# Performance work log

Measured on AMD Instinct MI355X. Metric: run time of the kernel, lower is better.

The kernel has to match this reference:

```python
import jax, jax.numpy as jnp
import numpy as np

B, T, N, PRED, DM = 16, 512, 128, 256, 32
L = T + PRED  # 768; conv windows 12 then 4: 768 -> 64 -> 16
EPS = 1e-5


def _conv1d(x, w, b, stride):
    # x: [B, C, L'], w: [C, C, k], kernel_size == stride, VALID (matches torch Conv1d)
    out = jax.lax.conv_general_dilated(x, w, (stride,), 'VALID',
                                       dimension_numbers=('NCH', 'OIH', 'NCH'))
    return out + b[None, :, None]


def _conv2d(x, w, b, pad):
    out = jax.lax.conv_general_dilated(x, w, (1, 1), [(pad, pad), (pad, pad)],
                                       dimension_numbers=('NCHW', 'OIHW', 'NCHW'))
    return out + b[None, :, None, None]


def _bn1d(x, g, b):
    # BatchNorm1d, training-mode batch statistics over (batch, length) per channel
    mu = x.mean((0, 2), keepdims=True)
    var = ((x - mu) ** 2).mean((0, 2), keepdims=True)
    return (x - mu) * jax.lax.rsqrt(var + EPS) * g[None, :, None] + b[None, :, None]


def _cubic_spline(y, size):
    # Natural cubic spline through values y: [B, Lk, C] at knots t = linspace(0,1,Lk),
    # evaluated at linspace(0,1,size). Natural BC: second derivative M=0 at endpoints.
    Bb, Lk, C = y.shape
    h = 1.0 / (Lk - 1)
    # tridiagonal system for interior second derivatives (uniform knots):
    # M[i-1] + 4 M[i] + M[i+1] = 6 * (y[i+1] - 2 y[i] + y[i-1]) / h^2
    m = Lk - 2
    rhs = (y[:, 2:, :] - 2.0 * y[:, 1:-1, :] + y[:, :-2, :]) * (6.0 / (h * h))  # [B,m,C]
    A = 4.0 * jnp.eye(m, dtype=y.dtype) + jnp.eye(m, k=1, dtype=y.dtype) + jnp.eye(m, k=-1, dtype=y.dtype)
    Mi = jnp.linalg.solve(A, rhs.transpose(1, 0, 2).reshape(m, Bb * C))  # [m, B*C]
    Mi = Mi.reshape(m, Bb, C).transpose(1, 0, 2)
    M = jnp.pad(Mi, ((0, 0), (1, 1), (0, 0)))  # [B, Lk, C], M[0]=M[-1]=0
    q = jnp.linspace(0.0, 1.0, size).astype(y.dtype)
    idx = jnp.clip(jnp.floor(q * (Lk - 1)).astype(jnp.int32), 0, Lk - 2)  # [size]
    s = (q - idx.astype(y.dtype) * h)[None, :, None]  # offset within interval
    u = h - s
    yi, yi1 = y[:, idx, :], y[:, idx + 1, :]
    M0, M1 = M[:, idx, :], M[:, idx + 1, :]
    hh6 = h * h / 6.0
    return ((M0 * u ** 3 + M1 * s ** 3) / (6.0 * h)
            + (yi - M0 * hh6) * (u / h)
            + (yi1 - M1 * hh6) * (s / h))  # [B, size, C]


def _forward(batch_x, le_w, le_b, c1_w, c1_b, bn1_g, bn1_b, c2_w, c2_b, bn2_g, bn2_b,
             i1_w0, i1_b0, i1_w1, i1_b1, i2_w0, i2_b0, i2_w1, i2_b1, ld_w, ld_b):
    # instance norm over time
    means = batch_x.mean(1, keepdims=True)
    xc = batch_x - means
    stdev = jnp.sqrt(xc.var(axis=1, keepdims=True) + EPS)
    xn = xc / stdev                               # [B, T, N]
    x = xn.transpose(0, 2, 1)                     # [B, N, T]
    x = jnp.einsum('bnt,lt->bnl', x, le_w) + le_b  # length_encoder -> [B, N, L]
    # multi-scale downsampling conv + spline back up to L
    scales = []
    t = x
    for win, cw, cb, g, bb in ((12, c1_w, c1_b, bn1_g, bn1_b), (4, c2_w, c2_b, bn2_g, bn2_b)):
        t = jax.nn.elu(_bn1d(_conv1d(t, cw, cb, win), g, bb))      # [B, N, L//...]
        scales.append(_cubic_spline(t.transpose(0, 2, 1), L).transpose(0, 2, 1))  # [B, N, L]
    a = jnp.stack([x] + scales, axis=1).transpose(0, 1, 3, 2)  # [B, 3, L, N]
    # Inception block 1 (num_kernels=2: 1x1 and 3x3, averaged), Dropout(eval)=id, GELU(exact)
    h1 = 0.5 * (_conv2d(a, i1_w0, i1_b0, 0) + _conv2d(a, i1_w1, i1_b1, 1))  # [B, DM, L, N]
    h1 = jax.nn.gelu(h1, approximate=False)
    # Inception block 2 -> 1 channel
    h2 = 0.5 * (_conv2d(h1, i2_w0, i2_b0, 0) + _conv2d(h1, i2_w1, i2_b1, 1))  # [B, 1, L, N]
    co = x + h2[:, 0].transpose(0, 2, 1)          # residual, [B, N, L]
    f = jnp.einsum('bnl,pl->bnp', co, ld_w) + ld_b  # length_decoder -> [B, N, PRED]
    f = f.transpose(0, 2, 1)                      # [B, PRED, N]
    return f * stdev[:, 0, :][:, None, :] + means[:, 0, :][:, None, :]


def setup_inputs():
    key = jax.random.key(0)
    ks = jax.random.split(key, 20)
    def w(i, shape, scale=0.02):
        return scale * jax.random.normal(ks[i], shape, jnp.float32)
    return dict(
        batch_x=jax.random.normal(ks[0], (B, T, N), jnp.float32),
        batch_x_mark=jax.random.normal(ks[1], (B, T, 4), jnp.float32),
        dec_inp=jax.random.normal(ks[2], (B, PRED, N), jnp.float32),
        batch_y_mark=jax.random.normal(ks[3], (B, PRED, 4), jnp.float32),
        le_w=w(4, (L, T)), le_b=w(5, (L,)),
        c1_w=w(6, (N, N, 12)), c1_b=w(7, (N,)),
        bn1_g=jnp.ones((N,), jnp.float32), bn1_b=jnp.zeros((N,), jnp.float32),
        c2_w=w(8, (N, N, 4)), c2_b=w(9, (N,)),
        bn2_g=jnp.ones((N,), jnp.float32), bn2_b=jnp.zeros((N,), jnp.float32),
        i1_w0=w(10, (DM, 3, 1, 1), 0.1), i1_b0=jnp.zeros((DM,), jnp.float32),
        i1_w1=w(11, (DM, 3, 3, 3), 0.1), i1_b1=jnp.zeros((DM,), jnp.float32),
        i2_w0=w(12, (1, DM, 1, 1), 0.1), i2_b0=jnp.zeros((1,), jnp.float32),
        i2_w1=w(13, (1, DM, 3, 3), 0.1), i2_b1=jnp.zeros((1,), jnp.float32),
        ld_w=w(14, (PRED, L)), ld_b=w(15, (PRED,)),
    )


def reference(batch_x, batch_x_mark, dec_inp, batch_y_mark, le_w, le_b,
              c1_w, c1_b, bn1_g, bn1_b, c2_w, c2_b, bn2_g, bn2_b,
              i1_w0, i1_b0, i1_w1, i1_b1, i2_w0, i2_b0, i2_w1, i2_b1, ld_w, ld_b):
    # batch_x_mark / dec_inp / batch_y_mark are accepted but unused (as in the torch forward)
    return _forward(batch_x, le_w, le_b, c1_w, c1_b, bn1_g, bn1_b, c2_w, c2_b, bn2_g, bn2_b,
                    i1_w0, i1_b0, i1_w1, i1_b1, i2_w0, i2_b0, i2_w1, i2_b1, ld_w, ld_b)
```

## Files before the change

kernel.cpp:

```cpp
#include <hip/hip_runtime.h>
#include <hip/hip_bf16.h>
#include <math.h>

#define BB 16
#define TT 512
#define NN 128
#define PREDN 256
#define DMC 32
#define LL 768
constexpr float EPSF = 1e-5f;
using bf16 = __hip_bfloat16;
using frag_ab = __attribute__((ext_vector_type(8))) short;
using frag_cd = __attribute__((ext_vector_type(4))) float;

__device__ __forceinline__ unsigned pbf2(float a, float b){
  union { bf16 h; unsigned short u; } x, y;
  x.h = __float2bfloat16(a); y.h = __float2bfloat16(b);
  return (unsigned)x.u | ((unsigned)y.u << 16);
}

__device__ __forceinline__ unsigned short bf16b(float v){
  union { bf16 h; unsigned short u; } x;
  x.h = __float2bfloat16(v);
  return x.u;
}

__device__ __forceinline__ float gelu_fast(float s){
  float s2v = s*s;
  float e = exp2f(s*fmaf(s2v, 0.10294396f, 2.30211806f));
  return s*e*__builtin_amdgcn_rcpf(e + 1.f);
}

__global__ void k_pre(const float* __restrict__ bx, const float* __restrict__ v0,
                      const float* __restrict__ v1, const float* __restrict__ w1c,
                      const float* __restrict__ w2c, const float* __restrict__ w0s1,
                      const float* __restrict__ w1s1, const float* __restrict__ b0s1,
                      const float* __restrict__ b1s1, const float* __restrict__ lew,
                      const float* __restrict__ ldw,
                      float* __restrict__ sp, float* __restrict__ s2p,
                      float* __restrict__ wT1, float* __restrict__ wT2,
                      uint4* __restrict__ bwpk, uint4* __restrict__ awpk,
                      float* __restrict__ bsum, unsigned* __restrict__ lewbf,
                      unsigned* __restrict__ ldwbf){
  int blk = blockIdx.x;
  if(blk < 64){
    int b = blk >> 2, tq = blk & 3, n = threadIdx.x;
    const float* p = bx + (size_t)b*TT*NN + (size_t)tq*128*NN + n;
    float s = 0.f, s2 = 0.f;
    for(int t=0;t<128;t++){ float v = p[(size_t)t*NN]; s += v; s2 += v*v; }
    sp[tq*2048 + b*NN + n] = s;
    s2p[tq*2048 + b*NN + n] = s2;
  } else if(blk < 192){
    int o = blk - 64;
    for(int k=threadIdx.x; k<1536; k+=blockDim.x)
      wT1[(size_t)k*NN + o] = w1c[(size_t)o*1536 + k];
  } else if(blk < 320){
    int o = blk - 192;
    for(int k=threadIdx.x; k<512; k+=blockDim.x)
      wT2[(size_t)k*NN + o] = w2c[(size_t)o*512 + k];
  } else if(blk == 320){
    int i = threadIdx.x;
    {
      int c = i >> 2, kq = i & 3;
      float w8[8];
      #pragma unroll
      for(int j=0;j<8;j++){
        int k = kq*8+j; float w = 0.f;
        if(k < 27){
          int ci = k/9, r9 = k - ci*9, dy = r9/3, dx = r9 - dy*3;
          w = 0.5f*w1s1[((c*3+ci)*3+dy)*3+dx];
          if(dy==1 && dx==1) w += 0.5f*w0s1[c*3+ci];
        }
        w8[j] = w;
      }
      bwpk[i] = make_uint4(pbf2(w8[0],w8[1]), pbf2(w8[2],w8[3]),
                           pbf2(w8[4],w8[5]), pbf2(w8[6],w8[7]));
    }
    if(i < 36){
      int tap = i >> 2, qq = i & 3, c8 = qq*8;
      float w8[8];
      #pragma unroll
      for(int j=0;j<8;j++){
        int c = c8 + j;
        w8[j] = 0.5f*v1[c*9 + tap] + ((tap==4) ? 0.5f*v0[c] : 0.f);
      }
      awpk[i] = make_uint4(pbf2(w8[0],w8[1]), pbf2(w8[2],w8[3]),
                           pbf2(w8[4],w8[5]), pbf2(w8[6],w8[7]));
    }
    if(i < 32) bsum[i] = 0.5f*(b0s1[i] + b1s1[i]);
  } else if(blk < 449){
    int o = blk - 321;
    for(int i=threadIdx.x; i<1536; i+=128){
      int l = o*6 + i/256, tp = i%256;
      lewbf[(size_t)l*256 + tp] = pbf2(lew[(size_t)l*TT + 2*tp], lew[(size_t)l*TT + 2*tp + 1]);
    }
  } else {
    int o = blk - 449;
    for(int i=threadIdx.x; i<1536; i+=128){
      int p = o*4 + i/384, tp = i%384;
      ldwbf[(size_t)p*384 + tp] = pbf2(ldw[(size_t)p*LL + 2*tp], ldw[(size_t)p*LL + 2*tp + 1]);
    }
  }
}

__global__ void k_musd(const float* __restrict__ sp, const float* __restrict__ s2p,
                       float* __restrict__ mu, float* __restrict__ rs){
  int i = blockIdx.x*256 + threadIdx.x;
  float ss = 0.f, s2 = 0.f;
  #pragma unroll
  for(int tq=0;tq<4;tq++){ ss += sp[tq*2048 + i]; s2 += s2p[tq*2048 + i]; }
  float m = ss*(1.f/512.f);
  mu[i] = m;
  rs[i] = 1.f/sqrtf(fmaxf(s2*(1.f/512.f) - m*m, 0.f) + EPSF);
}

__global__ __launch_bounds__(256) void k_xbf(const float* __restrict__ bx, const float* __restrict__ mu,
                                             const float* __restrict__ rs, unsigned short* __restrict__ xbf){
  int idx = blockIdx.x*256 + threadIdx.x;
  int ng = idx & 15, t = (idx >> 4) & 511, b = idx >> 13;
  int n8 = ng*8;
  const float* p = bx + ((size_t)b*TT + t)*NN + n8;
  float4 va = *(const float4*)p, vb2 = *(const float4*)(p+4);
  const float* mp = mu + b*NN + n8;
  const float* rp = rs + b*NN + n8;
  float4 m0 = *(const float4*)mp, m1 = *(const float4*)(mp+4);
  float4 r0 = *(const float4*)rp, r1 = *(const float4*)(rp+4);
  uint4 o;
  o.x = pbf2((va.x - m0.x)*r0.x, (va.y - m0.y)*r0.y);
  o.y = pbf2((va.z - m0.z)*r0.z, (va.w - m0.w)*r0.w);
  o.z = pbf2((vb2.x - m1.x)*r1.x, (vb2.y - m1.y)*r1.y);
  o.w = pbf2((vb2.z - m1.z)*r1.z, (vb2.w - m1.w)*r1.w);
  *(uint4*)&xbf[((size_t)b*TT + t)*NN + n8] = o;
}

__global__ __launch_bounds__(256) void k_gemm1(const unsigned short* __restrict__ xbf,
    const unsigned* __restrict__ lewbf, const float* __restrict__ leb,
    float* __restrict__ x, float* __restrict__ a0){
  __shared__ unsigned Asu[64*20];
  __shared__ unsigned Bsu[64*20];
  int tid = threadIdx.x;
  int row0 = blockIdx.x*64, l0 = blockIdx.y*64;
  int b = row0 >> 7, n0 = row0 & 127;
  int lane = tid & 63, wv = tid >> 6;
  frag_cd acc[4] = {};
  int an = tid & 63, akq = (tid >> 6)*8;
  int btk = tid & 15, blc = tid >> 4;
  unsigned ra[4], rbq[4];
  #pragma unroll
  for(int u=0;u<4;u++){
    unsigned lo = xbf[((size_t)b*TT + akq + 2*u)*NN + n0 + an];
    unsigned hi = xbf[((size_t)b*TT + akq + 2*u + 1)*NN + n0 + an];
    ra[u] = lo | (hi << 16);
    rbq[u] = lewbf[(size_t)(l0 + blc + 16*u)*256 + btk];
  }
  int fr = wv*16 + (lane & 15);
  int fq = (lane >> 4)*4;
  for(int k0=0;k0<TT;k0+=32){
    *(uint4*)&Asu[an*20 + (akq>>1)] = make_uint4(ra[0], ra[1], ra[2], ra[3]);
    #pragma unroll
    for(int p=0;p<4;p++) Bsu[(blc + 16*p)*20 + btk] = rbq[p];
    __syncthreads();
    if(k0 + 32 < TT){
      #pragma unroll
      for(int u=0;u<4;u++){
        unsigned lo = xbf[((size_t)b*TT + k0 + 32 + akq + 2*u)*NN + n0 + an];
        unsigned hi = xbf[((size_t)b*TT + k0 + 32 + akq + 2*u + 1)*NN + n0 + an];
        ra[u] = lo | (hi << 16);
        rbq[u] = lewbf[(size_t)(l0 + blc + 16*u)*256 + ((k0 + 32) >> 1) + btk];
      }
    }
    frag_ab af = *(const frag_ab*)&Asu[fr*20 + fq];
    #pragma unroll
    for(int nt=0;nt<4;nt++){
      frag_ab bf = *(const frag_ab*)&Bsu[(nt*16 + (lane & 15))*20 + fq];
      acc[nt] = __builtin_amdgcn_mfma_f32_16x16x32_bf16(af, bf, acc[nt], 0, 0, 0);
    }
    __syncthreads();
  }
  int col = lane & 15, quad = lane >> 4;
  #pragma unroll
  for(int nt=0;nt<4;nt++){
    int l = l0 + nt*16 + col;
    float lb = leb[l];
    #pragma unroll
    for(int r=0;r<4;r++){
      int m = wv*16 + quad*4 + r;
      x[(size_t)(row0 + m)*LL + l] = acc[nt][r] + lb;
    }
    float4 st;
    st.x = acc[nt][0] + lb;
    st.y = acc[nt][1] + lb;
    st.z = acc[nt][2] + lb;
    st.w = acc[nt][3] + lb;
    *(float4*)&a0[((size_t)b*LL + l)*NN + n0 + wv*16 + quad*4] = st;
  }
}

__global__ __launch_bounds__(512) void k_conv1(const float* __restrict__ x, const float* __restrict__ wT,
                                               const float* __restrict__ bias, float* __restrict__ t1){
  __shared__ alignas(16) float xs[NN*48];
  int jt = blockIdx.x, b = blockIdx.y;
  int tid = threadIdx.x;
  int o = tid & 127, jj = tid >> 7;
  for(int i=tid;i<NN*48;i+=512){
    int ci = i/48, kk = i%48;
    xs[i] = x[((size_t)b*NN + ci)*LL + jt*48 + kk];
  }
  __syncthreads();
  float a0 = 0.f, a1 = 0.f, a2 = 0.f, a3 = 0.f;
  for(int ci=0;ci<NN;ci++){
    const float* xc = xs + ci*48 + jj*12;
    const float* wc = wT + (size_t)(ci*12)*NN + o;
    #pragma unroll
    for(int kk=0;kk<12;kk+=4){
      a0 = fmaf(xc[kk+0], wc[(size_t)(kk+0)*NN], a0);
      a1 = fmaf(xc[kk+1], wc[(size_t)(kk+1)*NN], a1);
      a2 = fmaf(xc[kk+2], wc[(size_t)(kk+2)*NN], a2);
      a3 = fmaf(xc[kk+3], wc[(size_t)(kk+3)*NN], a3);
    }
  }
  int j = jt*4 + jj;
  t1[((size_t)b*NN + o)*64 + j] = (a0 + a1) + (a2 + a3) + bias[o];
}

__global__ void k_bnstats(const float* __restrict__ t, const float* __restrict__ g, const float* __restrict__ bb,
                          int Bcnt, int Jcnt, float* __restrict__ scale, float* __restrict__ shift){
  int o = blockIdx.x;
  int tot = Bcnt*Jcnt;
  float s = 0.f, s2 = 0.f;
  for(int i=threadIdx.x; i<tot; i+=blockDim.x){
    int b = i / Jcnt, j = i % Jcnt;
    float v = t[((size_t)b*NN + o)*Jcnt + j];
    s += v; s2 += v*v;
  }
  __shared__ float rs[256], rs2[256];
  rs[threadIdx.x] = s; rs2[threadIdx.x] = s2;
  __syncthreads();
  for(int st=128; st>0; st>>=1){
    if(threadIdx.x < st){ rs[threadIdx.x] += rs[threadIdx.x+st]; rs2[threadIdx.x] += rs2[threadIdx.x+st]; }
    __syncthreads();
  }
  if(threadIdx.x == 0){
    float mu = rs[0]/tot;
    float var = fmaxf(rs2[0]/tot - mu*mu, 0.f);
    float sc = g[o] * rsqrtf(var + EPSF);
    scale[o] = sc; shift[o] = bb[o] - mu*sc;
  }
}

__global__ void k_bnelu_t(const float* __restrict__ t, const float* __restrict__ scale,
                          const float* __restrict__ shift, int Jcnt, float* __restrict__ tt){
  int j = blockIdx.x, b = blockIdx.y, o = threadIdx.x;
  float v = t[((size_t)b*NN + o)*Jcnt + j]*scale[o] + shift[o];
  v = v > 0.f ? v : (expf(v) - 1.f);
  tt[((size_t)b*Jcnt + j)*NN + o] = v;
}

template<int LK>
__global__ void k_spline_solve(const float* __restrict__ y, float* __restrict__ M){
  constexpr int m = LK-2;
  const float Kc = 6.f*(LK-1)*(LK-1);
  __shared__ float cp[m];
  __shared__ float dp[m][NN];
  int b = blockIdx.x, c = threadIdx.x;
  if(c == 0){
    float cv = 0.25f; cp[0] = cv;
    for(int i=1;i<m;i++){ cv = 1.f/(4.f - cv); cp[i] = cv; }
  }
  __syncthreads();
  const float* yb = y + (size_t)b*LK*NN + c;
  float y0 = yb[0], y1 = yb[NN];
  float dprev = 0.f;
  for(int i=0;i<m;i++){
    float y2 = yb[(size_t)(i+2)*NN];
    float r = (y2 - 2.f*y1 + y0)*Kc;
    float d = (i == 0) ? r*0.25f : (r - dprev)*cp[i];
    dp[i][c] = d; dprev = d;
    y0 = y1; y1 = y2;
  }
  float* Mb = M + (size_t)b*LK*NN + c;
  float xv = dp[m-1][c];
  Mb[(size_t)m*NN] = xv;
  for(int i=m-2;i>=0;i--){
    xv = dp[i][c] - cp[i]*xv;
    Mb[(size_t)(i+1)*NN] = xv;
  }
  Mb[0] = 0.f;
  Mb[(size_t)(LK-1)*NN] = 0.f;
}

__device__ __forceinline__ float spline_pt(const float* __restrict__ y, const float* __restrict__ M,
                                           int LK, int l, int b, int c){
  float hh = 1.f/(LK-1);
  float q = (float)l * (1.f/(LL-1));
  int idx = (int)floorf(q*(LK-1));
  if(idx > LK-2) idx = LK-2;
  float s = q - idx*hh;
  float u = hh - s;
  const float* yb = y + ((size_t)b*LK + idx)*NN + c;
  const float* Mb = M + ((size_t)b*LK + idx)*NN + c;
  float yi = yb[0], yi1 = yb[NN], M0 = Mb[0], M1 = Mb[NN];
  float hh6 = hh*hh/6.f;
  return (M0*u*u*u + M1*s*s*s)*(1.f/(6.f*hh))
       + (yi  - M0*hh6)*(u*(1.f/hh))
       + (yi1 - M1*hh6)*(s*(1.f/hh));
}

__global__ __launch_bounds__(512) void k_conv2(const float* __restrict__ tt, const float* __restrict__ wT,
                                               const float* __restrict__ bias, float* __restrict__ t2){
  __shared__ alignas(16) float ts[16*NN];
  int jt = blockIdx.x, b = blockIdx.y;
  int tid = threadIdx.x;
  int o = tid & 127, jj = tid >> 7;
  for(int i=tid;i<16*NN;i+=512)
    ts[i] = tt[((size_t)b*64 + jt*16)*NN + i];
  __syncthreads();
  float a0 = 0.f, a1 = 0.f, a2 = 0.f, a3 = 0.f;
  for(int ci=0;ci<NN;ci++){
    const float* wc = wT + (size_t)(ci*4)*NN + o;
    const float* tc2 = ts + (jj*4)*NN + ci;
    a0 = fmaf(tc2[0*NN], wc[0*NN], a0);
    a1 = fmaf(tc2[1*NN], wc[1*NN], a1);
    a2 = fmaf(tc2[2*NN], wc[2*NN], a2);
    a3 = fmaf(tc2[3*NN], wc[3*NN], a3);
  }
  int j = jt*4 + jj;
  t2[((size_t)b*NN + o)*16 + j] = (a0 + a1) + (a2 + a3) + bias[o];
}

constexpr int KOFF[27] = {
    0,   1,   2,  36,  37,  38,  72,  73,  74,
  432, 433, 434, 468, 469, 470, 504, 505, 506,
  864, 865, 866, 900, 901, 902, 936, 937, 938
};

#define PBQ 1416
__global__ __launch_bounds__(256, 5) void k_h12(const float* __restrict__ a0,
    const float* __restrict__ y64, const float* __restrict__ M64,
    const float* __restrict__ y16, const float* __restrict__ M16,
    const uint4* __restrict__ bwpk, const uint4* __restrict__ awpk,
    const float* __restrict__ bsum, const float* __restrict__ vb0,
    const float* __restrict__ vb1, unsigned short* __restrict__ cobf){
  __shared__ alignas(16) unsigned short AsBf[3*12*36];
  __shared__ alignas(16) unsigned Au[4*PBQ];
  int tid = threadIdx.x;
  int l0 = blockIdx.x*8, n0 = blockIdx.y*32, b = blockIdx.z;
  int lane = tid & 63, wv = tid >> 6;
  int colB = lane & 15, qg = lane >> 4;

  for(int i=tid; i<648; i+=256){
    int ch = i/216, rem = i%216, yy = rem/18, xxp = rem%18;
    int xx = xxp*2;
    int gl = l0 + yy - 2, gn0 = n0 + xx - 2;
    float v0 = 0.f, v1 = 0.f;
    if(gl >= 0 && gl < LL){
      if(ch == 0){
        if((unsigned)gn0 < (unsigned)NN)     v0 = a0[((size_t)b*LL + gl)*NN + gn0];
        if((unsigned)(gn0+1) < (unsigned)NN) v1 = a0[((size_t)b*LL + gl)*NN + gn0 + 1];
      } else if(ch == 1){
        if((unsigned)gn0 < (unsigned)NN)     v0 = spline_pt(y64, M64, 64, gl, b, gn0);
        if((unsigned)(gn0+1) < (unsigned)NN) v1 = spline_pt(y64, M64, 64, gl, b, gn0+1);
      } else {
        if((unsigned)gn0 < (unsigned)NN)     v0 = spline_pt(y16, M16, 16, gl, b, gn0);
        if((unsigned)(gn0+1) < (unsigned)NN) v1 = spline_pt(y16, M16, 16, gl, b, gn0+1);
      }
    }
    *(unsigned*)&AsBf[i*2] = pbf2(v0, v1);
  }

  union U4 { uint4 q; frag_ab f; };
  U4 bw0, bw1;
  bw0.q = bwpk[colB*4 + qg];
  bw1.q = bwpk[(colB + 16)*4 + qg];
  float brA[4], brB[4];
  #pragma unroll
  for(int r=0;r<4;r++){ brA[r] = bsum[qg*4 + r]; brB[r] = bsum[16 + qg*4 + r]; }
  __syncthreads();

  for(int base=0; base<352; base+=128){
    int px = base + (tid >> 1);
    int half = tid & 1;
    if(px < 352){
      uint4 oA = make_uint4(0u,0u,0u,0u), oB = make_uint4(0u,0u,0u,0u);
      if(px < 340){
        int yy = px/34, xx = px - yy*34;
        const unsigned short* bp = AsBf + yy*36 + xx;
        if(half == 0){
          unsigned t0=bp[KOFF[0]],  t1=bp[KOFF[1]],  t2=bp[KOFF[2]],  t3=bp[KOFF[3]];
          unsigned t4=bp[KOFF[4]],  t5=bp[KOFF[5]],  t6=bp[KOFF[6]],  t7=bp[KOFF[7]];
          unsigned t8=bp[KOFF[8]],  t9=bp[KOFF[9]],  ta=bp[KOFF[10]], tb=bp[KOFF[11]];
          unsigned tc=bp[KOFF[12]], td=bp[KOFF[13]], te=bp[KOFF[14]], tf=bp[KOFF[15]];
          oA.x = t0 | (t1<<16); oA.y = t2 | (t3<<16); oA.z = t4 | (t5<<16); oA.w = t6 | (t7<<16);
          oB.x = t8 | (t9<<16); oB.y = ta | (tb<<16); oB.z = tc | (td<<16); oB.w = te | (tf<<16);
        } else {
          unsigned t0=bp[KOFF[16]], t1=bp[KOFF[17]], t2=bp[KOFF[18]], t3=bp[KOFF[19]];
          unsigned t4=bp[KOFF[20]], t5=bp[KOFF[21]], t6=bp[KOFF[22]], t7=bp[KOFF[23]];
          unsigned t8=bp[KOFF[24]], t9=bp[KOFF[25]], ta=bp[KOFF[26]];
          oA.x = t0 | (t1<<16); oA.y = t2 | (t3<<16); oA.z = t4 | (t5<<16); oA.w = t6 | (t7<<16);
          oB.x = t8 | (t9<<16); oB.y = ta;
        }
      }
      *(uint4*)&Au[(2*half)*PBQ + px*4]   = oA;
      *(uint4*)&Au[(2*half+1)*PBQ + px*4] = oB;
    }
  }
  __syncthreads();

  unsigned short* h1h = (unsigned short*)Au;
  frag_cd zac = {0.f, 0.f, 0.f, 0.f};
  for(int t = wv; t < 22; t += 4){
    int px = t*16 + colB;
    U4 av;
    av.q = *(const uint4*)&Au[qg*PBQ + px*4];
    frag_cd d0 = __builtin_amdgcn_mfma_f32_16x16x32_bf16(bw0.f, av.f, zac, 0, 0, 0);
    frag_cd d1 = __builtin_amdgcn_mfma_f32_16x16x32_bf16(bw1.f, av.f, zac, 0, 0, 0);
    unsigned u0 = pbf2(gelu_fast(d0[0] + brA[0]), gelu_fast(d0[1] + brA[1]));
    unsigned u1 = pbf2(gelu_fast(d0[2] + brA[2]), gelu_fast(d0[3] + brA[3]));
    unsigned u2 = pbf2(gelu_fast(d1[0] + brB[0]), gelu_fast(d1[1] + brB[1]));
    unsigned u3 = pbf2(gelu_fast(d1[2] + brB[2]), gelu_fast(d1[3] + brB[3]));
    int lo = (qg >> 1)*PBQ + px*4 + (qg & 1)*2;
    *(uint2*)&Au[lo]           = make_uint2(u0, u1);
    *(uint2*)&Au[2*PBQ + lo]   = make_uint2(u2, u3);
  }
  __syncthreads();

  if(n0 == 0){
    for(int i=tid;i<10*32;i+=256){ int yy=i>>5, ch=i&31;
      h1h[((ch>>3)*PBQ + (yy*34)*4)*2 + (ch&7)] = 0; }
  }
  if(n0 == 96){
    for(int i=tid;i<10*32;i+=256){ int yy=i>>5, ch=i&31;
      h1h[((ch>>3)*PBQ + (yy*34+33)*4)*2 + (ch&7)] = 0; }
  }
  if(l0 == 0){
    for(int i=tid;i<34*32;i+=256){ int xx=i>>5, ch=i&31;
      h1h[((ch>>3)*PBQ + xx*4)*2 + (ch&7)] = 0; }
  }
  if(l0 == 760){
    for(int i=tid;i<34*32;i+=256){ int xx=i>>5, ch=i&31;
      h1h[((ch>>3)*PBQ + (9*34+xx)*4)*2 + (ch&7)] = 0; }
  }

  U4 aw[9];
  #pragma unroll
  for(int tap=0; tap<9; tap++) aw[tap].q = awpk[tap*4 + qg];
  float vbsum = vb0[0] + vb1[0];
  __syncthreads();

  frag_cd cacc[4] = {};
  int baseoff[4];
  #pragma unroll
  for(int tt=0; tt<4; tt++){
    int px = (wv*4 + tt)*16 + colB;
    int yy = px >> 5, xx = px & 31;
    baseoff[tt] = qg*PBQ + (yy*34 + xx)*4;
  }
  #pragma unroll
  for(int dy=0; dy<3; dy++)
    #pragma unroll
    for(int dx=0; dx<3; dx++){
      int tap = dy*3 + dx;
      int off = (dy*34 + dx)*4;
      #pragma unroll
      for(int tt=0; tt<4; tt++){
        U4 bv;
        bv.q = *(const uint4*)&Au[baseoff[tt] + off];
        cacc[tt] = __builtin_amdgcn_mfma_f32_16x16x32_bf16(aw[tap].f, bv.f, cacc[tt], 0, 0, 0);
      }
    }
  if(lane < 16){
    #pragma unroll
    for(int tt=0; tt<4; tt++){
      int px = (wv*4 + tt)*16 + lane;
      int yy = px >> 5, xx = px & 31;
      size_t idx = ((size_t)b*LL + l0 + yy)*NN + n0 + xx;
      cobf[idx] = bf16b(cacc[tt][0] + vbsum + a0[idx]);
    }
  }
}

__global__ __launch_bounds__(256) void k_gemm2(const unsigned short* __restrict__ cobf,
    const unsigned* __restrict__ ldwbf, const float* __restrict__ ldb,
    const float* __restrict__ sp, const float* __restrict__ s2p,
    float* __restrict__ out){
  __shared__ unsigned Asu[64*20];
  __shared__ unsigned Bsu[32*20];
  int tid = threadIdx.x;
  int row0 = blockIdx.x*64, p0 = blockIdx.y*32;
  int b = row0 >> 7, n0 = row0 & 127;
  int lane = tid & 63, wv = tid >> 6;
  frag_cd acc[2] = {};
  int an = tid & 63, akq = (tid >> 6)*8;
  int btk = tid & 15, blc = tid >> 4;
  unsigned ra[4], rbq[2];
  #pragma unroll
  for(int u=0;u<4;u++){
    unsigned lo = cobf[((size_t)b*LL + akq + 2*u)*NN + n0 + an];
    unsigned hi = cobf[((size_t)b*LL + akq + 2*u + 1)*NN + n0 + an];
    ra[u] = lo | (hi << 16);
  }
  #pragma unroll
  for(int u=0;u<2;u++)
    rbq[u] = ldwbf[(size_t)(p0 + blc + 16*u)*384 + btk];
  int fr = wv*16 + (lane & 15);
  int fq = (lane >> 4)*4;
  for(int k0=0;k0<LL;k0+=32){
    *(uint4*)&Asu[an*20 + (akq>>1)] = make_uint4(ra[0], ra[1], ra[2], ra[3]);
    #pragma unroll
    for(int p=0;p<2;p++) Bsu[(blc + 16*p)*20 + btk] = rbq[p];
    __syncthreads();
    if(k0 + 32 < LL){
      #pragma unroll
      for(int u=0;u<4;u++){
        unsigned lo = cobf[((size_t)b*LL + k0 + 32 + akq + 2*u)*NN + n0 + an];
        unsigned hi = cobf[((size_t)b*LL + k0 + 32 + akq + 2*u + 1)*NN + n0 + an];
        ra[u] = lo | (hi << 16);
      }
      #pragma unroll
      for(int u=0;u<2;u++)
        rbq[u] = ldwbf[(size_t)(p0 + blc + 16*u)*384 + ((k0 + 32) >> 1) + btk];
    }
    frag_ab af = *(const frag_ab*)&Asu[fr*20 + fq];
    #pragma unroll
    for(int nt=0;nt<2;nt++){
      frag_ab bf = *(const frag_ab*)&Bsu[(nt*16 + (lane & 15))*20 + fq];
      acc[nt] = __builtin_amdgcn_mfma_f32_16x16x32_bf16(af, bf, acc[nt], 0, 0, 0);
    }
    __syncthreads();
  }
  int col = lane & 15, quad = lane >> 4;
  float mu_r[4], sd_r[4];
  #pragma unroll
  for(int r=0;r<4;r++){
    int row = row0 + wv*16 + quad*4 + r;
    float ssum = 0.f, s2sum = 0.f;
    #pragma unroll
    for(int tq=0;tq<4;tq++){ ssum += sp[tq*2048 + row]; s2sum += s2p[tq*2048 + row]; }
    float mu = ssum*(1.f/512.f);
    float var = fmaxf(s2sum*(1.f/512.f) - mu*mu, 0.f);
    mu_r[r] = mu; sd_r[r] = sqrtf(var + EPSF);
  }
  #pragma unroll
  for(int nt=0;nt<2;nt++){
    int p = p0 + nt*16 + col;
    float lb = ldb[p];
    float4 st;
    st.x = (acc[nt][0] + lb)*sd_r[0] + mu_r[0];
    st.y = (acc[nt][1] + lb)*sd_r[1] + mu_r[1];
    st.z = (acc[nt][2] + lb)*sd_r[2] + mu_r[2];
    st.w = (acc[nt][3] + lb)*sd_r[3] + mu_r[3];
    *(float4*)&out[((size_t)b*PREDN + p)*NN + n0 + wv*16 + quad*4] = st;
  }
}

extern "C" void kernel_launch(void* const* d_in, const int* in_sizes, int n_in,
                              void* d_out, int out_size, void* d_ws, size_t ws_size,
                              hipStream_t stream){
  (void)in_sizes; (void)n_in; (void)out_size; (void)ws_size;
  const float* batch_x = (const float*)d_in[0];
  const float* le_w  = (const float*)d_in[4];
  const float* le_b  = (const float*)d_in[5];
  const float* c1_w  = (const float*)d_in[6];
  const float* c1_b  = (const float*)d_in[7];
  const float* bn1_g = (const float*)d_in[8];
  const float* bn1_b = (const float*)d_in[9];
  const float* c2_w  = (const float*)d_in[10];
  const float* c2_b  = (const float*)d_in[11];
  const float* bn2_g = (const float*)d_in[12];
  const float* bn2_b = (const float*)d_in[13];
  const float* i1_w0 = (const float*)d_in[14];
  const float* i1_b0 = (const float*)d_in[15];
  const float* i1_w1 = (const float*)d_in[16];
  const float* i1_b1 = (const float*)d_in[17];
  const float* i2_w0 = (const float*)d_in[18];
  const float* i2_b0 = (const float*)d_in[19];
  const float* i2_w1 = (const float*)d_in[20];
  const float* i2_b1 = (const float*)d_in[21];
  const float* ld_w  = (const float*)d_in[22];
  const float* ld_b  = (const float*)d_in[23];
  float* out = (float*)d_out;

  float* ws   = (float*)d_ws;
  float* sp   = ws;
  float* s2p  = sp + 8192;
  float* wT1  = s2p + 8192;
  float* wT2  = wT1 + 196608;
  float* x    = wT2 + 65536;
  float* a0   = x + (size_t)BB*NN*LL;
  float* t1   = a0 + (size_t)BB*LL*NN;
  float* t1t  = t1 + (size_t)BB*NN*64;
  float* sc1  = t1t + (size_t)BB*64*NN;
  float* sh1  = sc1 + NN;
  float* Msp1 = sh1 + NN;
  float* t2   = Msp1 + (size_t)BB*64*NN;
  float* t2t  = t2 + (size_t)BB*NN*16;
  float* sc2  = t2t + (size_t)BB*16*NN;
  float* sh2  = sc2 + NN;
  float* Msp2 = sh2 + NN;
  float* muv  = Msp2 + (size_t)BB*16*NN;
  float* rsv  = muv + 2048;
  float* fB1  = rsv + 2048;
  unsigned short* xbf = (unsigned short*)fB1;
  float* fB2  = fB1 + 524288;
  unsigned* lewbf = (unsigned*)fB2;
  float* fB3  = fB2 + 196608;
  unsigned* ldwbf = (unsigned*)fB3;
  float* fB4  = fB3 + 98304;
  uint4* bwpk = (uint4*)fB4;
  float* fB5  = fB4 + 512;
  uint4* awpk = (uint4*)fB5;
  float* fB6  = fB5 + 144;
  float* bsum = fB6;
  float* fB7  = fB6 + 32;
  unsigned short* cobf = (unsigned short*)fB7;

  k_pre<<<513, 128, 0, stream>>>(batch_x, i2_w0, i2_w1, c1_w, c2_w,
                                 i1_w0, i1_w1, i1_b0, i1_b1, le_w, ld_w,
                                 sp, s2p, wT1, wT2, bwpk, awpk, bsum, lewbf, ldwbf);
  k_musd<<<8, 256, 0, stream>>>(sp, s2p, muv, rsv);
  k_xbf<<<512, 256, 0, stream>>>(batch_x, muv, rsv, xbf);
  k_gemm1<<<dim3(32,12), 256, 0, stream>>>(xbf, lewbf, le_b, x, a0);
  k_conv1<<<dim3(16,BB), 512, 0, stream>>>(x, wT1, c1_b, t1);
  k_bnstats<<<NN, 256, 0, stream>>>(t1, bn1_g, bn1_b, BB, 64, sc1, sh1);
  k_bnelu_t<<<dim3(64,BB), NN, 0, stream>>>(t1, sc1, sh1, 64, t1t);
  k_spline_solve<64><<<BB, NN, 0, stream>>>(t1t, Msp1);
  k_conv2<<<dim3(4,BB), 512, 0, stream>>>(t1t, wT2, c2_b, t2);
  k_bnstats<<<NN, 256, 0, stream>>>(t2, bn2_g, bn2_b, BB, 16, sc2, sh2);
  k_bnelu_t<<<dim3(16,BB), NN, 0, stream>>>(t2, sc2, sh2, 16, t2t);
  k_spline_solve<16><<<BB, NN, 0, stream>>>(t2t, Msp2);
  k_h12<<<dim3(96,4,BB), 256, 0, stream>>>(a0, t1t, Msp1, t2t, Msp2,
                                           bwpk, awpk, bsum, i2_b0, i2_b1, cobf);
  k_gemm2<<<dim3(32,8), 256, 0, stream>>>(cobf, ldwbf, ld_b, sp, s2p, out);
}
```

Baseline: 266.6 us.

## Fuse BN-ELU transpose into spline solve and restructure im2col packing

```diff
diff --git a/kernel.cpp b/kernel.cpp
--- a/kernel.cpp
+++ b/kernel.cpp
@@ -248,62 +248,78 @@
   }
 }
 
-__global__ void k_bnelu_t(const float* __restrict__ t, const float* __restrict__ scale,
-                          const float* __restrict__ shift, int Jcnt, float* __restrict__ tt){
-  int j = blockIdx.x, b = blockIdx.y, o = threadIdx.x;
-  float v = t[((size_t)b*NN + o)*Jcnt + j]*scale[o] + shift[o];
-  v = v > 0.f ? v : (expf(v) - 1.f);
-  tt[((size_t)b*Jcnt + j)*NN + o] = v;
-}
-
 template<int LK>
-__global__ void k_spline_solve(const float* __restrict__ y, float* __restrict__ M){
+__global__ __launch_bounds__(256) void k_bnspl(const float* __restrict__ t, const float* __restrict__ scale,
+    const float* __restrict__ shift, float* __restrict__ tt, float* __restrict__ M){
   constexpr int m = LK-2;
-  const float Kc = 6.f*(LK-1)*(LK-1);
+  __shared__ float yt[LK][NN+1];
   __shared__ float cp[m];
   __shared__ float dp[m][NN];
-  int b = blockIdx.x, c = threadIdx.x;
-  if(c == 0){
+  int b = blockIdx.x, tid = threadIdx.x;
+  for(int i=tid; i<LK*NN; i+=256){
+    int o = i / LK, j = i - o*LK;
+    float v = t[((size_t)b*NN + o)*LK + j]*scale[o] + shift[o];
+    v = v > 0.f ? v : (expf(v) - 1.f);
+    yt[j][o] = v;
+  }
+  if(tid == 0){
     float cv = 0.25f; cp[0] = cv;
     for(int i=1;i<m;i++){ cv = 1.f/(4.f - cv); cp[i] = cv; }
   }
   __syncthreads();
-  const float* yb = y + (size_t)b*LK*NN + c;
-  float y0 = yb[0], y1 = yb[NN];
-  float dprev = 0.f;
-  for(int i=0;i<m;i++){
-    float y2 = yb[(size_t)(i+2)*NN];
-    float r = (y2 - 2.f*y1 + y0)*Kc;
-    float d = (i == 0) ? r*0.25f : (r - dprev)*cp[i];
-    dp[i][c] = d; dprev = d;
-    y0 = y1; y1 = y2;
-  }
-  float* Mb = M + (size_t)b*LK*NN + c;
-  float xv = dp[m-1][c];
-  Mb[(size_t)m*NN] = xv;
-  for(int i=m-2;i>=0;i--){
-    xv = dp[i][c] - cp[i]*xv;
-    Mb[(size_t)(i+1)*NN] = xv;
-  }
-  Mb[0] = 0.f;
-  Mb[(size_t)(LK-1)*NN] = 0.f;
-}
-
-__device__ __forceinline__ float spline_pt(const float* __restrict__ y, const float* __restrict__ M,
-                                           int LK, int l, int b, int c){
-  float hh = 1.f/(LK-1);
+  for(int i=tid; i<LK*NN; i+=256){
+    int j = i >> 7, o = i & 127;
+    tt[((size_t)b*LK + j)*NN + o] = yt[j][o];
+  }
+  if(tid < NN){
+    int c = tid;
+    const float Kc = 6.f*(LK-1)*(LK-1);
+    float y0 = yt[0][c], y1 = yt[1][c];
+    float dprev = 0.f;
+    for(int i=0;i<m;i++){
+      float y2 = yt[i+2][c];
+      float r = (y2 - 2.f*y1 + y0)*Kc;
+      float d = (i == 0) ? r*0.25f : (r - dprev)*cp[i];
+      dp[i][c] = d; dprev = d;
+      y0 = y1; y1 = y2;
+    }
+    float* Mb = M + (size_t)b*LK*NN + c;
+    float xv = dp[m-1][c];
+    Mb[(size_t)m*NN] = xv;
+    for(int i=m-2;i>=0;i--){
+      xv = dp[i][c] - cp[i]*xv;
+      Mb[(size_t)(i+1)*NN] = xv;
+    }
+    Mb[0] = 0.f;
+    Mb[(size_t)(LK-1)*NN] = 0.f;
+  }
+}
+
+template<int LK>
+__device__ __forceinline__ void spline_pair(const float* __restrict__ y, const float* __restrict__ M,
+    int l, int b, int c0, bool ok0, bool ok1, float& v0, float& v1){
+  const float hh = 1.f/(LK-1);
   float q = (float)l * (1.f/(LL-1));
   int idx = (int)floorf(q*(LK-1));
   if(idx > LK-2) idx = LK-2;
   float s = q - idx*hh;
   float u = hh - s;
-  const float* yb = y + ((size_t)b*LK + idx)*NN + c;
-  const float* Mb = M + ((size_t)b*LK + idx)*NN + c;
-  float yi = yb[0], yi1 = yb[NN], M0 = Mb[0], M1 = Mb[NN];
-  float hh6 = hh*hh/6.f;
-  return (M0*u*u*u + M1*s*s*s)*(1.f/(6.f*hh))
-       + (yi  - M0*hh6)*(u*(1.f/hh))
-       + (yi1 - M1*hh6)*(s*(1.f/hh));
+  const float hh6 = hh*hh/6.f;
+  const float i6h = 1.f/(6.f*hh);
+  const float ih = 1.f/hh;
+  float cu = u*u*u, cs = s*s*s;
+  float uh = u*ih, sh = s*ih;
+  const float* yb = y + ((size_t)b*LK + idx)*NN + c0;
+  const float* Mb = M + ((size_t)b*LK + idx)*NN + c0;
+  v0 = 0.f; v1 = 0.f;
+  if(ok0){
+    float yi = yb[0], yi1 = yb[NN], M0 = Mb[0], M1 = Mb[NN];
+    v0 = (M0*cu + M1*cs)*i6h + (yi - M0*hh6)*uh + (yi1 - M1*hh6)*sh;
+  }
+  if(ok1){
+    float yi = yb[1], yi1 = yb[NN+1], M0 = Mb[1], M1 = Mb[NN+1];
+    v1 = (M0*cu + M1*cs)*i6h + (yi - M0*hh6)*uh + (yi1 - M1*hh6)*sh;
+  }
 }
 
 __global__ __launch_bounds__(512) void k_conv2(const float* __restrict__ tt, const float* __restrict__ wT,
@@ -327,12 +343,6 @@
   int j = jt*4 + jj;
   t2[((size_t)b*NN + o)*16 + j] = (a0 + a1) + (a2 + a3) + bias[o];
 }
-
-constexpr int KOFF[27] = {
-    0,   1,   2,  36,  37,  38,  72,  73,  74,
-  432, 433, 434, 468, 469, 470, 504, 505, 506,
-  864, 865, 866, 900, 901, 902, 936, 937, 938
-};
 
 #define PBQ 1416
 __global__ __launch_bounds__(256, 5) void k_h12(const float* __restrict__ a0,
@@ -352,18 +362,16 @@
     int ch = i/216, rem = i%216, yy = rem/18, xxp = rem%18;
     int xx = xxp*2;
     int gl = l0 + yy - 2, gn0 = n0 + xx - 2;
+    bool okl = (gl >= 0 && gl < LL);
+    bool ok0 = okl && ((unsigned)gn0 < (unsigned)NN);
+    bool ok1 = okl && ((unsigned)(gn0+1) < (unsigned)NN);
     float v0 = 0.f, v1 = 0.f;
-    if(gl >= 0 && gl < LL){
-      if(ch == 0){
-        if((unsigned)gn0 < (unsigned)NN)     v0 = a0[((size_t)b*LL + gl)*NN + gn0];
-        if((unsigned)(gn0+1) < (unsigned)NN) v1 = a0[((size_t)b*LL + gl)*NN + gn0 + 1];
-      } else if(ch == 1){
-        if((unsigned)gn0 < (unsigned)NN)     v0 = spline_pt(y64, M64, 64, gl, b, gn0);
-        if((unsigned)(gn0+1) < (unsigned)NN) v1 = spline_pt(y64, M64, 64, gl, b, gn0+1);
-      } else {
-        if((unsigned)gn0 < (unsigned)NN)     v0 = spline_pt(y16, M16, 16, gl, b, gn0);
-        if((unsigned)(gn0+1) < (unsigned)NN) v1 = spline_pt(y16, M16, 16, gl, b, gn0+1);
-      }
+    if(ch == 0){
+      if(ok0) v0 = a0[((size_t)b*LL + gl)*NN + gn0];
+      if(ok1) v1 = a0[((size_t)b*LL + gl)*NN + gn0 + 1];
+    } else if(okl){
+      if(ch == 1) spline_pair<64>(y64, M64, gl, b, gn0, ok0, ok1, v0, v1);
+      else        spline_pair<16>(y16, M16, gl, b, gn0, ok0, ok1, v0, v1);
     }
     *(unsigned*)&AsBf[i*2] = pbf2(v0, v1);
   }
@@ -377,31 +385,70 @@
   for(int r=0;r<4;r++){ brA[r] = bsum[qg*4 + r]; brB[r] = bsum[16 + qg*4 + r]; }
   __syncthreads();
 
-  for(int base=0; base<352; base+=128){
-    int px = base + (tid >> 1);
-    int half = tid & 1;
-    if(px < 352){
-      uint4 oA = make_uint4(0u,0u,0u,0u), oB = make_uint4(0u,0u,0u,0u);
-      if(px < 340){
-        int yy = px/34, xx = px - yy*34;
-        const unsigned short* bp = AsBf + yy*36 + xx;
-        if(half == 0){
-          unsigned t0=bp[KOFF[0]],  t1=bp[KOFF[1]],  t2=bp[KOFF[2]],  t3=bp[KOFF[3]];
-          unsigned t4=bp[KOFF[4]],  t5=bp[KOFF[5]],  t6=bp[KOFF[6]],  t7=bp[KOFF[7]];
-          unsigned t8=bp[KOFF[8]],  t9=bp[KOFF[9]],  ta=bp[KOFF[10]], tb=bp[KOFF[11]];
-          unsigned tc=bp[KOFF[12]], td=bp[KOFF[13]], te=bp[KOFF[14]], tf=bp[KOFF[15]];
-          oA.x = t0 | (t1<<16); oA.y = t2 | (t3<<16); oA.z = t4 | (t5<<16); oA.w = t6 | (t7<<16);
-          oB.x = t8 | (t9<<16); oB.y = ta | (tb<<16); oB.z = tc | (td<<16); oB.w = te | (tf<<16);
-        } else {
-          unsigned t0=bp[KOFF[16]], t1=bp[KOFF[17]], t2=bp[KOFF[18]], t3=bp[KOFF[19]];
-          unsigned t4=bp[KOFF[20]], t5=bp[KOFF[21]], t6=bp[KOFF[22]], t7=bp[KOFF[23]];
-          unsigned t8=bp[KOFF[24]], t9=bp[KOFF[25]], ta=bp[KOFF[26]];
-          oA.x = t0 | (t1<<16); oA.y = t2 | (t3<<16); oA.z = t4 | (t5<<16); oA.w = t6 | (t7<<16);
-          oB.x = t8 | (t9<<16); oB.y = ta;
+  {
+    const unsigned* Uv = (const unsigned*)AsBf;
+    if(tid < 176){
+      if(tid < 170){
+        int yy = tid/17, xp = tid - yy*17;
+        unsigned g[3][3][2];
+        #pragma unroll
+        for(int ci=0;ci<3;ci++)
+          #pragma unroll
+          for(int dy=0;dy<3;dy++){
+            int base = (ci*12 + yy + dy)*18 + xp;
+            g[ci][dy][0] = Uv[base];
+            g[ci][dy][1] = Uv[base+1];
+          }
+        int px0 = yy*34 + 2*xp;
+        uint4 pq;
+        pq.x = g[0][0][0];
+        pq.y = (g[0][0][1]&0xffffu) | (g[0][1][0]<<16);
+        pq.z = (g[0][1][0]>>16) | (g[0][1][1]<<16);
+        pq.w = g[0][2][0];
+        *(uint4*)&Au[0*PBQ + px0*4] = pq;
+        pq.x = (g[0][2][1]&0xffffu) | (g[1][0][0]<<16);
+        pq.y = (g[1][0][0]>>16) | (g[1][0][1]<<16);
+        pq.z = g[1][1][0];
+        pq.w = (g[1][1][1]&0xffffu) | (g[1][2][0]<<16);
+        *(uint4*)&Au[1*PBQ + px0*4] = pq;
+        pq.x = (g[1][2][0]>>16) | (g[1][2][1]<<16);
+        pq.y = g[2][0][0];
+        pq.z = (g[2][0][1]&0xffffu) | (g[2][1][0]<<16);
+        pq.w = (g[2][1][0]>>16) | (g[2][1][1]<<16);
+        *(uint4*)&Au[2*PBQ + px0*4] = pq;
+        pq.x = g[2][2][0];
+        pq.y = g[2][2][1]&0xffffu;
+        pq.z = 0u; pq.w = 0u;
+        *(uint4*)&Au[3*PBQ + px0*4] = pq;
+        int px1 = px0 + 1;
+        pq.x = (g[0][0][0]>>16) | (g[0][0][1]<<16);
+        pq.y = (g[0][0][1]>>16) | (g[0][1][0]&0xffff0000u);
+        pq.z = g[0][1][1];
+        pq.w = (g[0][2][0]>>16) | (g[0][2][1]<<16);
+        *(uint4*)&Au[0*PBQ + px1*4] = pq;
+        pq.x = (g[0][2][1]>>16) | (g[1][0][0]&0xffff0000u);
+        pq.y = g[1][0][1];
+        pq.z = (g[1][1][0]>>16) | (g[1][1][1]<<16);
+        pq.w = (g[1][1][1]>>16) | (g[1][2][0]&0xffff0000u);
+        *(uint4*)&Au[1*PBQ + px1*4] = pq;
+        pq.x = g[1][2][1];
+        pq.y = (g[2][0][0]>>16) | (g[2][0][1]<<16);
+        pq.z = (g[2][0][1]>>16) | (g[2][1][0]&0xffff0000u);
+        pq.w = g[2][1][1];
+        *(uint4*)&Au[2*PBQ + px1*4] = pq;
+        pq.x = (g[2][2][0]>>16) | (g[2][2][1]<<16);
+        pq.y = g[2][2][1]>>16;
+        pq.z = 0u; pq.w = 0u;
+        *(uint4*)&Au[3*PBQ + px1*4] = pq;
+      } else {
+        int px = 340 + (tid-170)*2;
+        uint4 z = make_uint4(0u,0u,0u,0u);
+        #pragma unroll
+        for(int q=0;q<4;q++){
+          *(uint4*)&Au[q*PBQ + px*4]     = z;
+          *(uint4*)&Au[q*PBQ + (px+1)*4] = z;
         }
       }
-      *(uint4*)&Au[(2*half)*PBQ + px*4]   = oA;
-      *(uint4*)&Au[(2*half+1)*PBQ + px*4] = oB;
     }
   }
   __syncthreads();
@@ -622,12 +669,10 @@
   k_gemm1<<<dim3(32,12), 256, 0, stream>>>(xbf, lewbf, le_b, x, a0);
   k_conv1<<<dim3(16,BB), 512, 0, stream>>>(x, wT1, c1_b, t1);
   k_bnstats<<<NN, 256, 0, stream>>>(t1, bn1_g, bn1_b, BB, 64, sc1, sh1);
-  k_bnelu_t<<<dim3(64,BB), NN, 0, stream>>>(t1, sc1, sh1, 64, t1t);
-  k_spline_solve<64><<<BB, NN, 0, stream>>>(t1t, Msp1);
+  k_bnspl<64><<<BB, 256, 0, stream>>>(t1, sc1, sh1, t1t, Msp1);
   k_conv2<<<dim3(4,BB), 512, 0, stream>>>(t1t, wT2, c2_b, t2);
   k_bnstats<<<NN, 256, 0, stream>>>(t2, bn2_g, bn2_b, BB, 16, sc2, sh2);
-  k_bnelu_t<<<dim3(16,BB), NN, 0, stream>>>(t2, sc2, sh2, 16, t2t);
-  k_spline_solve<16><<<BB, NN, 0, stream>>>(t2t, Msp2);
+  k_bnspl<16><<<BB, 256, 0, stream>>>(t2, sc2, sh2, t2t, Msp2);
   k_h12<<<dim3(96,4,BB), 256, 0, stream>>>(a0, t1t, Msp1, t2t, Msp2,
                                            bwpk, awpk, bsum, i2_b0, i2_b1, cobf);
   k_gemm2<<<dim3(32,8), 256, 0, stream>>>(cobf, ldwbf, ld_b, sp, s2p, out);
```

Measured after the change: 258.4 us. 1.03x faster.
